# Kernel tuning notes

Hardware: AMD Instinct MI355X
Metric: run time of the kernel (lower is better)

The kernel has to match this reference:

```python
import jax, jax.numpy as jnp
import numpy as np

B, S, D, H = 2, 2048, 1024, 16
HD = D // H  # 64
SCALE = float(np.sqrt(HD))


def setup_inputs() -> dict:
    key = jax.random.key(0)
    ks = jax.random.split(key, 11)
    def lin(kw, kb, fan_in):
        bound = 1.0 / np.sqrt(fan_in)
        W = jax.random.uniform(kw, (D, D), jnp.float32, -bound, bound)
        b = jax.random.uniform(kb, (D,), jnp.float32, -bound, bound)
        return W, b
    Wq, bq = lin(ks[0], ks[1], D)
    Wk, bk = lin(ks[2], ks[3], D)
    Wv, bv = lin(ks[4], ks[5], D)
    Wo, bo = lin(ks[6], ks[7], D)
    q = jax.random.normal(ks[8], (B, S, D), jnp.float32)
    k = jax.random.normal(ks[9], (B, S, D), jnp.float32)
    v = jax.random.normal(ks[10], (B, S, D), jnp.float32)
    mask = jnp.ones((B, 1, S, S), jnp.int32)
    return {"q": q, "k": k, "v": v, "mask": mask,
            "Wq": Wq, "bq": bq, "Wk": Wk, "bk": bk,
            "Wv": Wv, "bv": bv, "Wo": Wo, "bo": bo}


def reference(q, k, v, mask, Wq, bq, Wk, bk, Wv, bv, Wo, bo):
    # torch Linear: x @ W.T + b
    def proj(x, W, b):
        y = x @ W.T + b                      # [B,S,D]
        return y.reshape(B, -1, H, HD).transpose(0, 2, 1, 3)  # [B,H,S,HD]
    Q = proj(q, Wq, bq)
    K = proj(k, Wk, bk)
    V = proj(v, Wv, bv)
    scores = jnp.einsum('bhqd,bhkd->bhqk', Q, K) / SCALE     # [B,H,S,S]
    scores = jnp.where(mask == 0, -1e9, scores)
    attn = jax.nn.softmax(scores, axis=-1)                   # dropout in eval mode = identity
    out = jnp.einsum('bhqk,bhkd->bhqd', attn, V)             # [B,H,S,HD]
    out = out.transpose(0, 2, 1, 3).reshape(B, -1, D)        # [B,S,D]
    return out @ Wo.T + bo
```

## Files before the change

### kernel.cpp

```cpp
#include <hip/hip_runtime.h>
#include <math.h>

#define BB 2
#define SS 2048
#define DD 1024
#define HH 16
#define HDIM 64
#define KK 1024
#define MM 4096

#define QFOLD 0.18033688011112042f

typedef _Float16 f16x2 __attribute__((ext_vector_type(2)));
typedef _Float16 f16x4 __attribute__((ext_vector_type(4)));
typedef _Float16 f16x8 __attribute__((ext_vector_type(8)));
typedef float    f32x4 __attribute__((ext_vector_type(4)));

#define GLL16(gp, lp) __builtin_amdgcn_global_load_lds(                        \
    (const __attribute__((address_space(1))) void*)(gp),                       \
    (__attribute__((address_space(3))) void*)(lp), 16, 0, 0)

static __device__ __forceinline__ float fast_exp2(float x) {
    float r;
    asm("v_exp_f32 %0, %1" : "=v"(r) : "v"(x));
    return r;
}
static __device__ __forceinline__ f16x2 cvt_pk(float a, float b) {
    f16x2 r;
    asm("v_cvt_pkrtz_f16_f32 %0, %1, %2" : "=v"(r) : "v"(a), "v"(b));
    return r;
}

__global__ __launch_bounds__(256) void prep(
    const float* __restrict__ q,  const float* __restrict__ k,
    const float* __restrict__ v,  const float* __restrict__ wq,
    const float* __restrict__ wk, const float* __restrict__ wv,
    const float* __restrict__ wo, const int* __restrict__ mask,
    _Float16* __restrict__ qh,  _Float16* __restrict__ kh,
    _Float16* __restrict__ vh,  _Float16* __restrict__ wqh,
    _Float16* __restrict__ wkh, _Float16* __restrict__ wvh,
    _Float16* __restrict__ woh, unsigned short* __restrict__ bm16)
{
    if (blockIdx.x < 16384u) {
        const unsigned u  = blockIdx.x * 256u + threadIdx.x;
        const unsigned U1 = 1u << 20;
        const unsigned U2 = 1u << 18;
        const float* src; _Float16* dst; unsigned off;
        float sc = 1.0f;
        if (u < 3u * U1) {
            const unsigned t = u >> 20; off = u & (U1 - 1u);
            src = (t == 0) ? q  : (t == 1) ? k  : v;
            dst = (t == 0) ? qh : (t == 1) ? kh : vh;
        } else {
            const unsigned r = u - 3u * U1;
            const unsigned t = r >> 18; off = r & (U2 - 1u);
            src = (t == 0) ? wq  : (t == 1) ? wk  : (t == 2) ? wv  : wo;
            dst = (t == 0) ? wqh : (t == 1) ? wkh : (t == 2) ? wvh : woh;
            if (t == 0) sc = QFOLD;
        }
        const float4 x = ((const float4*)src)[off];
        f16x4 y;
        y[0] = (_Float16)(x.x * sc); y[1] = (_Float16)(x.y * sc);
        y[2] = (_Float16)(x.z * sc); y[3] = (_Float16)(x.w * sc);
        ((f16x4*)dst)[off] = y;
    } else {
        const size_t t = (size_t)(blockIdx.x - 16384u) * 256 + threadIdx.x;
        const int4* p = (const int4*)(mask + t * 16);
        const int4 a = p[0], b = p[1], c = p[2], d = p[3];
        unsigned vv = 0;
        vv |= (a.x != 0) << 0;  vv |= (a.y != 0) << 1;
        vv |= (a.z != 0) << 2;  vv |= (a.w != 0) << 3;
        vv |= (b.x != 0) << 4;  vv |= (b.y != 0) << 5;
        vv |= (b.z != 0) << 6;  vv |= (b.w != 0) << 7;
        vv |= (c.x != 0) << 8;  vv |= (c.y != 0) << 9;
        vv |= (c.z != 0) << 10; vv |= (c.w != 0) << 11;
        vv |= (d.x != 0) << 12; vv |= (d.y != 0) << 13;
        vv |= (d.z != 0) << 14; vv |= (d.w != 0) << 15;
        bm16[t] = (unsigned short)vv;
    }
}

#define GEMM_BODY(X, W)                                                        \
    __shared__ _Float16 As[128 * 32];                                          \
    __shared__ _Float16 Bs[64 * 32];                                           \
    const int tid  = threadIdx.x;                                              \
    const int lane = tid & 63;                                                 \
    const int lr   = lane & 15;                                                \
    const int lg   = lane >> 4;                                                \
    const int wave = tid >> 6;                                                 \
    const int wr   = wave >> 1;                                                \
    const int wc   = wave & 1;                                                 \
    const int m0 = blockIdx.y << 7;                                            \
    const int n0 = blockIdx.x << 6;                                            \
    const char* Xb = (const char*)(X);                                         \
    const char* Wb = (const char*)(W);                                         \
    const int pa0 = tid * 16;                                                  \
    const int pa1 = pa0 + 4096;                                                \
    const int ra0 = pa0 >> 6, ca0 = pa0 & 63;                                  \
    const int ra1 = pa1 >> 6, ca1 = pa1 & 63;                                  \
    const int rb0 = pa0 >> 6, cb0 = pa0 & 63;                                  \
    f32x4 acc[4][2] = {};                                                      \
    for (int k0 = 0; k0 < KK; k0 += 32) {                                      \
        GLL16(Xb + ((size_t)(m0 + ra0) * KK + k0) * 2 + ca0, (char*)As + pa0); \
        GLL16(Xb + ((size_t)(m0 + ra1) * KK + k0) * 2 + ca1, (char*)As + pa1); \
        GLL16(Wb + ((size_t)(n0 + rb0) * KK + k0) * 2 + cb0, (char*)Bs + pa0); \
        __syncthreads();                                                       \
        f16x8 af[4], bf[2];                                                    \
        _Pragma("unroll")                                                      \
        for (int mi = 0; mi < 4; ++mi)                                         \
            af[mi] = *(const f16x8*)((const char*)As +                         \
                       ((wr * 64 + mi * 16 + lr) * 64 + lg * 16));             \
        _Pragma("unroll")                                                      \
        for (int ni = 0; ni < 2; ++ni)                                         \
            bf[ni] = *(const f16x8*)((const char*)Bs +                         \
                       ((wc * 32 + ni * 16 + lr) * 64 + lg * 16));             \
        _Pragma("unroll")                                                      \
        for (int mi = 0; mi < 4; ++mi)                                         \
            _Pragma("unroll")                                                  \
            for (int ni = 0; ni < 2; ++ni)                                     \
                acc[mi][ni] = __builtin_amdgcn_mfma_f32_16x16x32_f16(          \
                    af[mi], bf[ni], acc[mi][ni], 0, 0, 0);                     \
        __syncthreads();                                                       \
    }

__global__ __launch_bounds__(256) void gemm_qkv(
    const _Float16* __restrict__ qx, const _Float16* __restrict__ kx,
    const _Float16* __restrict__ vx,
    const _Float16* __restrict__ wqh, const _Float16* __restrict__ wkh,
    const _Float16* __restrict__ wvh,
    const float* __restrict__ bq, const float* __restrict__ bk,
    const float* __restrict__ bv,
    _Float16* __restrict__ Qh, _Float16* __restrict__ Kh,
    _Float16* __restrict__ Vt)
{
    const int z = blockIdx.z;
    const _Float16* X = (z == 0) ? qx : (z == 1) ? kx : vx;
    const _Float16* W = (z == 0) ? wqh : (z == 1) ? wkh : wvh;
    const float* bias = (z == 0) ? bq : (z == 1) ? bk : bv;
    const float bsc   = (z == 0) ? QFOLD : 1.0f;
    _Float16* Yh      = (z == 0) ? Qh : Kh;

    GEMM_BODY(X, W)

    #pragma unroll
    for (int ni = 0; ni < 2; ++ni) {
        const int n  = n0 + wc * 32 + ni * 16 + lr;
        const float bv_ = bias[n] * bsc;
        #pragma unroll
        for (int mi = 0; mi < 4; ++mi) {
            const int mbase = m0 + wr * 64 + mi * 16 + lg * 4;
            if (z < 2) {
                #pragma unroll
                for (int r = 0; r < 4; ++r) {
                    const int m = mbase + r;
                    const int b_ = m >> 11, s_ = m & (SS - 1);
                    const int h_ = n >> 6,  d_ = n & (HDIM - 1);
                    Yh[(((size_t)(b_ * HH + h_)) * SS + s_) * HDIM + d_] =
                        (_Float16)(acc[mi][ni][r] + bv_);
                }
            } else {
                const int b_ = mbase >> 11, s_ = mbase & (SS - 1);
                const int h_ = n >> 6,      d_ = n & (HDIM - 1);
                f16x4 tv;
                #pragma unroll
                for (int r = 0; r < 4; ++r) tv[r] = (_Float16)(acc[mi][ni][r] + bv_);
                *(f16x4*)(Vt + (((size_t)(b_ * HH + h_)) * HDIM + d_) * SS + s_) = tv;
            }
        }
    }
}

__global__ __launch_bounds__(256) void gemm_out(
    const _Float16* __restrict__ X, const _Float16* __restrict__ W,
    const float* __restrict__ bias, float* __restrict__ Y)
{
    GEMM_BODY(X, W)

    #pragma unroll
    for (int ni = 0; ni < 2; ++ni) {
        const int n  = n0 + wc * 32 + ni * 16 + lr;
        const float bv_ = bias[n];
        #pragma unroll
        for (int mi = 0; mi < 4; ++mi) {
            const int mbase = m0 + wr * 64 + mi * 16 + lg * 4;
            #pragma unroll
            for (int r = 0; r < 4; ++r)
                Y[(size_t)(mbase + r) * DD + n] = acc[mi][ni][r] + bv_;
        }
    }
}

__global__ __launch_bounds__(256) void attn_mfma4(
    const _Float16* __restrict__ Qh, const _Float16* __restrict__ Kh,
    const _Float16* __restrict__ Vt, const unsigned long long* __restrict__ bm,
    _Float16* __restrict__ AO)
{
    __shared__ _Float16 KbufS[2][4096];
    __shared__ _Float16 VbufS[2][4096];

    const int tid  = threadIdx.x;
    const int lane = tid & 63;
    const int wq   = tid >> 6;
    const int bh   = blockIdx.x;
    const int b_   = bh >> 4;
    const int h_   = bh & (HH - 1);
    const int q0   = blockIdx.y << 7;
    const int lr   = lane & 15;
    const int lg   = lane >> 4;

    const int qrowA = q0 + wq * 32 + lr;
    const int qrowB = qrowA + 16;
    const _Float16* qbA = Qh + ((size_t)bh * SS + qrowA) * HDIM;
    const _Float16* qbB = Qh + ((size_t)bh * SS + qrowB) * HDIM;
    const f16x8 qfA0 = *(const f16x8*)(qbA + lg * 8);
    const f16x8 qfA1 = *(const f16x8*)(qbA + 32 + lg * 8);
    const f16x8 qfB0 = *(const f16x8*)(qbB + lg * 8);
    const f16x8 qfB1 = *(const f16x8*)(qbB + 32 + lg * 8);

    const int c0 = tid, c1 = tid + 256;
    const int kr0 = c0 >> 3, krc0 = (c0 & 7) ^ (kr0 & 7);
    const int kr1 = c1 >> 3, krc1 = (c1 & 7) ^ (kr1 & 7);
    const _Float16* gK0 = Kh + ((size_t)bh * SS + kr0) * HDIM + krc0 * 8;
    const _Float16* gK1 = Kh + ((size_t)bh * SS + kr1) * HDIM + krc1 * 8;
    const _Float16* gV0 = Vt + ((size_t)bh * HDIM + kr0) * SS + krc0 * 8;
    const _Float16* gV1 = Vt + ((size_t)bh * HDIM + kr1) * SS + krc1 * 8;
    const int woff = (tid >> 6) << 10;

    float mA = -INFINITY, mB = -INFINITY;
    f32x4 oaccA[4], oaccB[4];
    #pragma unroll
    for (int dc = 0; dc < 4; ++dc) {
        oaccA[dc] = (f32x4){0.f, 0.f, 0.f, 0.f};
        oaccB[dc] = (f32x4){0.f, 0.f, 0.f, 0.f};
    }
    f32x4 laccA = (f32x4){0.f, 0.f, 0.f, 0.f};
    f32x4 laccB = (f32x4){0.f, 0.f, 0.f, 0.f};

    f16x8 ones;
    #pragma unroll
    for (int e = 0; e < 8; ++e) ones[e] = (_Float16)1.0f;

    const unsigned long long* bmrowA = bm + ((size_t)b_ * SS + qrowA) * (SS / 64);
    const unsigned long long* bmrowB = bm + ((size_t)b_ * SS + qrowB) * (SS / 64);

#define STAGE(KT, BSEL) do {                                                   \
    GLL16(gK0 + (size_t)(KT) * HDIM, (char*)KbufS[BSEL] + woff);               \
    GLL16(gK1 + (size_t)(KT) * HDIM, (char*)KbufS[BSEL] + 4096 + woff);        \
    GLL16(gV0 + (KT), (char*)VbufS[BSEL] + woff);                              \
    GLL16(gV1 + (KT), (char*)VbufS[BSEL] + 4096 + woff);                       \
  } while (0)

    STAGE(0, 0);
    __syncthreads();

    const int xk0 = ((lg       ^ (lr & 7)) << 4);
    const int xk1 = (((4 + lg) ^ (lr & 7)) << 4);
    const int xv  = ((lr & 7) << 4);

    unsigned long long bmA = bmrowA[0];
    unsigned long long bmB = bmrowB[0];

    for (int t = 0; t < SS / 64; ++t) {
        const int cur = t & 1;
        if (t < SS / 64 - 1) STAGE((t + 1) * 64, cur ^ 1);
        unsigned long long bmA_n = 0, bmB_n = 0;
        if (t < SS / 64 - 1) { bmA_n = bmrowA[t + 1]; bmB_n = bmrowB[t + 1]; }

        const char* kb = (const char*)KbufS[cur];
        const char* vb = (const char*)VbufS[cur];

        f32x4 sA[4], sB[4];
        __builtin_amdgcn_s_setprio(1);
        #pragma unroll
        for (int kg = 0; kg < 4; ++kg) {
            const char* rp = kb + (kg * 16 + lr) * 128;
            const f16x8 kf0 = *(const f16x8*)(rp + xk0);
            const f16x8 kf1 = *(const f16x8*)(rp + xk1);
            f32x4 a = (f32x4){0.f, 0.f, 0.f, 0.f};
            a = __builtin_amdgcn_mfma_f32_16x16x32_f16(kf0, qfA0, a, 0, 0, 0);
            a = __builtin_amdgcn_mfma_f32_16x16x32_f16(kf1, qfA1, a, 0, 0, 0);
            sA[kg] = a;
            f32x4 b2 = (f32x4){0.f, 0.f, 0.f, 0.f};
            b2 = __builtin_amdgcn_mfma_f32_16x16x32_f16(kf0, qfB0, b2, 0, 0, 0);
            b2 = __builtin_amdgcn_mfma_f32_16x16x32_f16(kf1, qfB1, b2, 0, 0, 0);
            sB[kg] = b2;
        }
        __builtin_amdgcn_s_setprio(0);

        float svA[16], svB[16];
        #pragma unroll
        for (int kg = 0; kg < 4; ++kg)
            #pragma unroll
            for (int r = 0; r < 4; ++r) {
                svA[kg * 4 + r] = sA[kg][r];
                svB[kg * 4 + r] = sB[kg][r];
            }

        if (~bmA) {
            #pragma unroll
            for (int kg = 0; kg < 4; ++kg)
                #pragma unroll
                for (int r = 0; r < 4; ++r)
                    if (!((bmA >> (kg * 16 + lg * 4 + r)) & 1ull))
                        svA[kg * 4 + r] = -1e9f;
        }
        if (~bmB) {
            #pragma unroll
            for (int kg = 0; kg < 4; ++kg)
                #pragma unroll
                for (int r = 0; r < 4; ++r)
                    if (!((bmB >> (kg * 16 + lg * 4 + r)) & 1ull))
                        svB[kg * 4 + r] = -1e9f;
        }
        bmA = bmA_n; bmB = bmB_n;

        float pmA = svA[0], pmB = svB[0];
        #pragma unroll
        for (int i = 1; i < 16; ++i) {
            pmA = fmaxf(pmA, svA[i]);
            pmB = fmaxf(pmB, svB[i]);
        }
        pmA = fmaxf(pmA, __shfl_xor(pmA, 16));
        pmA = fmaxf(pmA, __shfl_xor(pmA, 32));
        pmB = fmaxf(pmB, __shfl_xor(pmB, 16));
        pmB = fmaxf(pmB, __shfl_xor(pmB, 32));

        if (!__all(pmA <= mA + 8.0f)) {
            const float m_new = fmaxf(mA, pmA);
            const float corr  = fast_exp2(mA - m_new);
            #pragma unroll
            for (int dc = 0; dc < 4; ++dc) oaccA[dc] *= corr;
            laccA *= corr;
            mA = m_new;
        }
        if (!__all(pmB <= mB + 8.0f)) {
            const float m_new = fmaxf(mB, pmB);
            const float corr  = fast_exp2(mB - m_new);
            #pragma unroll
            for (int dc = 0; dc < 4; ++dc) oaccB[dc] *= corr;
            laccB *= corr;
            mB = m_new;
        }

        float pA[16], pB[16];
        #pragma unroll
        for (int i = 0; i < 16; ++i) {
            pA[i] = fast_exp2(svA[i] - mA);
            pB[i] = fast_exp2(svB[i] - mB);
        }

        union { f16x2 h2[4]; f16x8 v8; } uA0, uA1, uB0, uB1;
        #pragma unroll
        for (int e = 0; e < 4; ++e) {
            uA0.h2[e] = cvt_pk(pA[2 * e],     pA[2 * e + 1]);
            uA1.h2[e] = cvt_pk(pA[8 + 2 * e], pA[9 + 2 * e]);
            uB0.h2[e] = cvt_pk(pB[2 * e],     pB[2 * e + 1]);
            uB1.h2[e] = cvt_pk(pB[8 + 2 * e], pB[9 + 2 * e]);
        }
        const f16x8 pbA0 = uA0.v8, pbA1 = uA1.v8;
        const f16x8 pbB0 = uB0.v8, pbB1 = uB1.v8;

        __builtin_amdgcn_s_setprio(1);
        #pragma unroll
        for (int dc = 0; dc < 4; ++dc) {
            const char* rp = vb + (dc * 16 + lr) * 128;
            const f16x4 a0 = *(const f16x4*)(rp + ((0  + lg * 8) ^ xv));
            const f16x4 a1 = *(const f16x4*)(rp + ((32 + lg * 8) ^ xv));
            const f16x4 a2 = *(const f16x4*)(rp + ((64 + lg * 8) ^ xv));
            const f16x4 a3 = *(const f16x4*)(rp + ((96 + lg * 8) ^ xv));
            const f16x8 va0 = __builtin_shufflevector(a0, a1, 0, 1, 2, 3, 4, 5, 6, 7);
            const f16x8 va1 = __builtin_shufflevector(a2, a3, 0, 1, 2, 3, 4, 5, 6, 7);
            oaccA[dc] = __builtin_amdgcn_mfma_f32_16x16x32_f16(va0, pbA0, oaccA[dc], 0, 0, 0);
            oaccA[dc] = __builtin_amdgcn_mfma_f32_16x16x32_f16(va1, pbA1, oaccA[dc], 0, 0, 0);
            oaccB[dc] = __builtin_amdgcn_mfma_f32_16x16x32_f16(va0, pbB0, oaccB[dc], 0, 0, 0);
            oaccB[dc] = __builtin_amdgcn_mfma_f32_16x16x32_f16(va1, pbB1, oaccB[dc], 0, 0, 0);
        }
        laccA = __builtin_amdgcn_mfma_f32_16x16x32_f16(ones, pbA0, laccA, 0, 0, 0);
        laccA = __builtin_amdgcn_mfma_f32_16x16x32_f16(ones, pbA1, laccA, 0, 0, 0);
        laccB = __builtin_amdgcn_mfma_f32_16x16x32_f16(ones, pbB0, laccB, 0, 0, 0);
        laccB = __builtin_amdgcn_mfma_f32_16x16x32_f16(ones, pbB1, laccB, 0, 0, 0);
        __builtin_amdgcn_s_setprio(0);
        __syncthreads();
    }
#undef STAGE

    const float invlA = 1.0f / laccA[0];
    const float invlB = 1.0f / laccB[0];
    _Float16* obA = AO + ((size_t)b_ * SS + qrowA) * DD + h_ * HDIM;
    _Float16* obB = AO + ((size_t)b_ * SS + qrowB) * DD + h_ * HDIM;
    #pragma unroll
    for (int dc = 0; dc < 4; ++dc) {
        f16x4 rA, rB;
        #pragma unroll
        for (int r = 0; r < 4; ++r) {
            rA[r] = (_Float16)(oaccA[dc][r] * invlA);
            rB[r] = (_Float16)(oaccB[dc][r] * invlB);
        }
        *reinterpret_cast<f16x4*>(obA + dc * 16 + lg * 4) = rA;
        *reinterpret_cast<f16x4*>(obB + dc * 16 + lg * 4) = rB;
    }
}

extern "C" void kernel_launch(void* const* d_in, const int* in_sizes, int n_in,
                              void* d_out, int out_size, void* d_ws, size_t ws_size,
                              hipStream_t stream)
{
    const float* q    = (const float*)d_in[0];
    const float* k    = (const float*)d_in[1];
    const float* v    = (const float*)d_in[2];
    const int*   mask = (const int*)d_in[3];
    const float* Wq   = (const float*)d_in[4];
    const float* bq   = (const float*)d_in[5];
    const float* Wk   = (const float*)d_in[6];
    const float* bk   = (const float*)d_in[7];
    const float* Wv   = (const float*)d_in[8];
    const float* bv   = (const float*)d_in[9];
    const float* Wo   = (const float*)d_in[10];
    const float* bo   = (const float*)d_in[11];
    float* out = (float*)d_out;

    char* w = (char*)d_ws;
    _Float16* qx  = (_Float16*)(w);
    _Float16* kx  = (_Float16*)(w + 8  * 1048576);
    _Float16* vx  = (_Float16*)(w + 16 * 1048576);
    _Float16* wqh = (_Float16*)(w + 24 * 1048576);
    _Float16* wkh = (_Float16*)(w + 26 * 1048576);
    _Float16* wvh = (_Float16*)(w + 28 * 1048576);
    _Float16* woh = (_Float16*)(w + 30 * 1048576);
    _Float16* Qh  = (_Float16*)(w + 32 * 1048576);
    _Float16* Kh  = (_Float16*)(w + 40 * 1048576);
    _Float16* Vt  = (_Float16*)(w + 48 * 1048576);
    unsigned long long* bm = (unsigned long long*)(w + 56 * 1048576);
    _Float16* AO  = (_Float16*)(w);

    prep<<<18432, 256, 0, stream>>>(q, k, v, Wq, Wk, Wv, Wo, mask,
                                    qx, kx, vx, wqh, wkh, wvh, woh,
                                    (unsigned short*)bm);

    const dim3 gqkv(DD / 64, MM / 128, 3);
    gemm_qkv<<<gqkv, 256, 0, stream>>>(qx, kx, vx, wqh, wkh, wvh,
                                       bq, bk, bv, Qh, Kh, Vt);

    const dim3 gattn(BB * HH, SS / 128);
    attn_mfma4<<<gattn, 256, 0, stream>>>(Qh, Kh, Vt, bm, AO);

    const dim3 gout(DD / 64, MM / 128);
    gemm_out<<<gout, 256, 0, stream>>>(AO, woh, bo, out);
}
```

Before: 167.6 us.

## Split attention key range across two blocks and merge with log-sum-exp combine kernel

```diff
diff --git a/kernel.cpp b/kernel.cpp
--- a/kernel.cpp
+++ b/kernel.cpp
@@ -8,6 +8,7 @@
 #define HDIM 64
 #define KK 1024
 #define MM 4096
+#define KSPLIT 2
 
 #define QFOLD 0.18033688011112042f
 
@@ -23,6 +24,11 @@
 static __device__ __forceinline__ float fast_exp2(float x) {
     float r;
     asm("v_exp_f32 %0, %1" : "=v"(r) : "v"(x));
+    return r;
+}
+static __device__ __forceinline__ float fast_log2(float x) {
+    float r;
+    asm("v_log_f32 %0, %1" : "=v"(r) : "v"(x));
     return r;
 }
 static __device__ __forceinline__ f16x2 cvt_pk(float a, float b) {
@@ -190,10 +196,10 @@
     }
 }
 
-__global__ __launch_bounds__(256) void attn_mfma4(
+__global__ __launch_bounds__(256) void attn_mfma5(
     const _Float16* __restrict__ Qh, const _Float16* __restrict__ Kh,
     const _Float16* __restrict__ Vt, const unsigned long long* __restrict__ bm,
-    _Float16* __restrict__ AO)
+    _Float16* __restrict__ Opart, float* __restrict__ Lpart)
 {
     __shared__ _Float16 KbufS[2][4096];
     __shared__ _Float16 VbufS[2][4096];
@@ -203,10 +209,13 @@
     const int wq   = tid >> 6;
     const int bh   = blockIdx.x;
     const int b_   = bh >> 4;
-    const int h_   = bh & (HH - 1);
     const int q0   = blockIdx.y << 7;
+    const int ks   = blockIdx.z;
     const int lr   = lane & 15;
     const int lg   = lane >> 4;
+
+    const int NT = SS / 64 / KSPLIT;
+    const int t0 = ks * NT;
 
     const int qrowA = q0 + wq * 32 + lr;
     const int qrowB = qrowA + 16;
@@ -250,21 +259,22 @@
     GLL16(gV1 + (KT), (char*)VbufS[BSEL] + 4096 + woff);                       \
   } while (0)
 
-    STAGE(0, 0);
+    STAGE(t0 * 64, 0);
     __syncthreads();
 
     const int xk0 = ((lg       ^ (lr & 7)) << 4);
     const int xk1 = (((4 + lg) ^ (lr & 7)) << 4);
     const int xv  = ((lr & 7) << 4);
 
-    unsigned long long bmA = bmrowA[0];
-    unsigned long long bmB = bmrowB[0];
-
-    for (int t = 0; t < SS / 64; ++t) {
-        const int cur = t & 1;
-        if (t < SS / 64 - 1) STAGE((t + 1) * 64, cur ^ 1);
+    unsigned long long bmA = bmrowA[t0];
+    unsigned long long bmB = bmrowB[t0];
+
+    for (int ti = 0; ti < NT; ++ti) {
+        const int t = t0 + ti;
+        const int cur = ti & 1;
+        if (ti < NT - 1) STAGE((t + 1) * 64, cur ^ 1);
         unsigned long long bmA_n = 0, bmB_n = 0;
-        if (t < SS / 64 - 1) { bmA_n = bmrowA[t + 1]; bmB_n = bmrowB[t + 1]; }
+        if (ti < NT - 1) { bmA_n = bmrowA[t + 1]; bmB_n = bmrowB[t + 1]; }
 
         const char* kb = (const char*)KbufS[cur];
         const char* vb = (const char*)VbufS[cur];
@@ -384,10 +394,16 @@
     }
 #undef STAGE
 
+    _Float16* Op = Opart + (size_t)ks * (BB * HH) * SS * HDIM;
+    float*    Lp = Lpart + (size_t)ks * (BB * HH) * SS;
+
     const float invlA = 1.0f / laccA[0];
     const float invlB = 1.0f / laccB[0];
-    _Float16* obA = AO + ((size_t)b_ * SS + qrowA) * DD + h_ * HDIM;
-    _Float16* obB = AO + ((size_t)b_ * SS + qrowB) * DD + h_ * HDIM;
+    const float LA_ = mA + fast_log2(laccA[0]);
+    const float LB_ = mB + fast_log2(laccB[0]);
+
+    _Float16* opA = Op + ((size_t)bh * SS + qrowA) * HDIM;
+    _Float16* opB = Op + ((size_t)bh * SS + qrowB) * HDIM;
     #pragma unroll
     for (int dc = 0; dc < 4; ++dc) {
         f16x4 rA, rB;
@@ -396,9 +412,39 @@
             rA[r] = (_Float16)(oaccA[dc][r] * invlA);
             rB[r] = (_Float16)(oaccB[dc][r] * invlB);
         }
-        *reinterpret_cast<f16x4*>(obA + dc * 16 + lg * 4) = rA;
-        *reinterpret_cast<f16x4*>(obB + dc * 16 + lg * 4) = rB;
-    }
+        *reinterpret_cast<f16x4*>(opA + dc * 16 + lg * 4) = rA;
+        *reinterpret_cast<f16x4*>(opB + dc * 16 + lg * 4) = rB;
+    }
+    if (lg == 0) {
+        Lp[(size_t)bh * SS + qrowA] = LA_;
+        Lp[(size_t)bh * SS + qrowB] = LB_;
+    }
+}
+
+__global__ __launch_bounds__(256) void combine(
+    const _Float16* __restrict__ Opart, const float* __restrict__ Lpart,
+    _Float16* __restrict__ AO)
+{
+    const int tid = threadIdx.x;
+    const int row = blockIdx.x * 32 + (tid >> 3);
+    const int dc  = (tid & 7) * 8;
+    const int bh = row >> 11, s = row & (SS - 1);
+    const int b_ = bh >> 4,   h_ = bh & (HH - 1);
+    const size_t PER = (size_t)(BB * HH) * SS;
+
+    const float L0 = Lpart[row], L1 = Lpart[PER + row];
+    const float Ls = fmaxf(L0, L1);
+    const float w0 = fast_exp2(L0 - Ls);
+    const float w1 = fast_exp2(L1 - Ls);
+    const float inv = 1.0f / (w0 + w1);
+
+    const f16x8 a = *(const f16x8*)(Opart + (size_t)row * HDIM + dc);
+    const f16x8 b = *(const f16x8*)(Opart + PER * HDIM + (size_t)row * HDIM + dc);
+    f16x8 r;
+    #pragma unroll
+    for (int i = 0; i < 8; ++i)
+        r[i] = (_Float16)(((float)a[i] * w0 + (float)b[i] * w1) * inv);
+    *(f16x8*)(AO + ((size_t)b_ * SS + s) * DD + h_ * HDIM + dc) = r;
 }
 
 extern "C" void kernel_launch(void* const* d_in, const int* in_sizes, int n_in,
@@ -431,7 +477,9 @@
     _Float16* Kh  = (_Float16*)(w + 40 * 1048576);
     _Float16* Vt  = (_Float16*)(w + 48 * 1048576);
     unsigned long long* bm = (unsigned long long*)(w + 56 * 1048576);
-    _Float16* AO  = (_Float16*)(w);
+    _Float16* Opart = (_Float16*)(w + 8 * 1048576);
+    float*    Lpart = (float*)(w + 24 * 1048576);
+    _Float16* AO    = (_Float16*)(w);
 
     prep<<<18432, 256, 0, stream>>>(q, k, v, Wq, Wk, Wv, Wo, mask,
                                     qx, kx, vx, wqh, wkh, wvh, woh,
@@ -441,8 +489,10 @@
     gemm_qkv<<<gqkv, 256, 0, stream>>>(qx, kx, vx, wqh, wkh, wvh,
                                        bq, bk, bv, Qh, Kh, Vt);
 
-    const dim3 gattn(BB * HH, SS / 128);
-    attn_mfma4<<<gattn, 256, 0, stream>>>(Qh, Kh, Vt, bm, AO);
+    const dim3 gattn(BB * HH, SS / 128, KSPLIT);
+    attn_mfma5<<<gattn, 256, 0, stream>>>(Qh, Kh, Vt, bm, Opart, Lpart);
+
+    combine<<<2048, 256, 0, stream>>>(Opart, Lpart, AO);
 
     const dim3 gout(DD / 64, MM / 128);
     gemm_out<<<gout, 256, 0, stream>>>(AO, woh, bo, out);
```

Result: slower. 175.5 us (+4.7%).

## Switch attention kernel to 32x32x16 MFMA tiles with permlane32 P-fragment reshuffle

Applied to the files above, without the earlier changes.

```diff
diff --git a/kernel.cpp b/kernel.cpp
--- a/kernel.cpp
+++ b/kernel.cpp
@@ -15,6 +15,8 @@
 typedef _Float16 f16x4 __attribute__((ext_vector_type(4)));
 typedef _Float16 f16x8 __attribute__((ext_vector_type(8)));
 typedef float    f32x4 __attribute__((ext_vector_type(4)));
+typedef float    f32x16 __attribute__((ext_vector_type(16)));
+typedef unsigned uint2v __attribute__((ext_vector_type(2)));
 
 #define GLL16(gp, lp) __builtin_amdgcn_global_load_lds(                        \
     (const __attribute__((address_space(1))) void*)(gp),                       \
@@ -25,10 +27,10 @@
     asm("v_exp_f32 %0, %1" : "=v"(r) : "v"(x));
     return r;
 }
-static __device__ __forceinline__ f16x2 cvt_pk(float a, float b) {
-    f16x2 r;
-    asm("v_cvt_pkrtz_f16_f32 %0, %1, %2" : "=v"(r) : "v"(a), "v"(b));
-    return r;
+static __device__ __forceinline__ unsigned cvt_pk_u(float a, float b) {
+    union { f16x2 h; unsigned u; } r;
+    asm("v_cvt_pkrtz_f16_f32 %0, %1, %2" : "=v"(r.h) : "v"(a), "v"(b));
+    return r.u;
 }
 
 __global__ __launch_bounds__(256) void prep(
@@ -190,7 +192,7 @@
     }
 }
 
-__global__ __launch_bounds__(256) void attn_mfma4(
+__global__ __launch_bounds__(256) void attn_mfma7(
     const _Float16* __restrict__ Qh, const _Float16* __restrict__ Kh,
     const _Float16* __restrict__ Vt, const unsigned long long* __restrict__ bm,
     _Float16* __restrict__ AO)
@@ -205,17 +207,15 @@
     const int b_   = bh >> 4;
     const int h_   = bh & (HH - 1);
     const int q0   = blockIdx.y << 7;
-    const int lr   = lane & 15;
-    const int lg   = lane >> 4;
-
-    const int qrowA = q0 + wq * 32 + lr;
-    const int qrowB = qrowA + 16;
-    const _Float16* qbA = Qh + ((size_t)bh * SS + qrowA) * HDIM;
-    const _Float16* qbB = Qh + ((size_t)bh * SS + qrowB) * HDIM;
-    const f16x8 qfA0 = *(const f16x8*)(qbA + lg * 8);
-    const f16x8 qfA1 = *(const f16x8*)(qbA + 32 + lg * 8);
-    const f16x8 qfB0 = *(const f16x8*)(qbB + lg * 8);
-    const f16x8 qfB1 = *(const f16x8*)(qbB + 32 + lg * 8);
+    const int lq   = lane & 31;
+    const int hi   = lane >> 5;
+
+    const int qrow = q0 + wq * 32 + lq;
+    const _Float16* qbase = Qh + ((size_t)bh * SS + qrow) * HDIM;
+    f16x8 qf[4];
+    #pragma unroll
+    for (int j = 0; j < 4; ++j)
+        qf[j] = *(const f16x8*)(qbase + j * 16 + hi * 8);
 
     const int c0 = tid, c1 = tid + 256;
     const int kr0 = c0 >> 3, krc0 = (c0 & 7) ^ (kr0 & 7);
@@ -226,22 +226,12 @@
     const _Float16* gV1 = Vt + ((size_t)bh * HDIM + kr1) * SS + krc1 * 8;
     const int woff = (tid >> 6) << 10;
 
-    float mA = -INFINITY, mB = -INFINITY;
-    f32x4 oaccA[4], oaccB[4];
+    float m_run = -INFINITY, l_run = 0.f;
+    f32x16 oacc0, oacc1;
     #pragma unroll
-    for (int dc = 0; dc < 4; ++dc) {
-        oaccA[dc] = (f32x4){0.f, 0.f, 0.f, 0.f};
-        oaccB[dc] = (f32x4){0.f, 0.f, 0.f, 0.f};
-    }
-    f32x4 laccA = (f32x4){0.f, 0.f, 0.f, 0.f};
-    f32x4 laccB = (f32x4){0.f, 0.f, 0.f, 0.f};
-
-    f16x8 ones;
-    #pragma unroll
-    for (int e = 0; e < 8; ++e) ones[e] = (_Float16)1.0f;
-
-    const unsigned long long* bmrowA = bm + ((size_t)b_ * SS + qrowA) * (SS / 64);
-    const unsigned long long* bmrowB = bm + ((size_t)b_ * SS + qrowB) * (SS / 64);
+    for (int i = 0; i < 16; ++i) { oacc0[i] = 0.f; oacc1[i] = 0.f; }
+
+    const unsigned long long* bmrow = bm + ((size_t)b_ * SS + qrow) * (SS / 64);
 
 #define STAGE(KT, BSEL) do {                                                   \
     GLL16(gK0 + (size_t)(KT) * HDIM, (char*)KbufS[BSEL] + woff);               \
@@ -253,151 +243,115 @@
     STAGE(0, 0);
     __syncthreads();
 
-    const int xk0 = ((lg       ^ (lr & 7)) << 4);
-    const int xk1 = (((4 + lg) ^ (lr & 7)) << 4);
-    const int xv  = ((lr & 7) << 4);
-
-    unsigned long long bmA = bmrowA[0];
-    unsigned long long bmB = bmrowB[0];
+    const int kxor = lq & 7;
+    unsigned long long bmv = bmrow[0];
 
     for (int t = 0; t < SS / 64; ++t) {
         const int cur = t & 1;
         if (t < SS / 64 - 1) STAGE((t + 1) * 64, cur ^ 1);
-        unsigned long long bmA_n = 0, bmB_n = 0;
-        if (t < SS / 64 - 1) { bmA_n = bmrowA[t + 1]; bmB_n = bmrowB[t + 1]; }
+        unsigned long long bmv_n = 0;
+        if (t < SS / 64 - 1) bmv_n = bmrow[t + 1];
 
         const char* kb = (const char*)KbufS[cur];
         const char* vb = (const char*)VbufS[cur];
 
-        f32x4 sA[4], sB[4];
+        f32x16 s0, s1;
+        #pragma unroll
+        for (int i = 0; i < 16; ++i) { s0[i] = 0.f; s1[i] = 0.f; }
         __builtin_amdgcn_s_setprio(1);
         #pragma unroll
-        for (int kg = 0; kg < 4; ++kg) {
-            const char* rp = kb + (kg * 16 + lr) * 128;
-            const f16x8 kf0 = *(const f16x8*)(rp + xk0);
-            const f16x8 kf1 = *(const f16x8*)(rp + xk1);
-            f32x4 a = (f32x4){0.f, 0.f, 0.f, 0.f};
-            a = __builtin_amdgcn_mfma_f32_16x16x32_f16(kf0, qfA0, a, 0, 0, 0);
-            a = __builtin_amdgcn_mfma_f32_16x16x32_f16(kf1, qfA1, a, 0, 0, 0);
-            sA[kg] = a;
-            f32x4 b2 = (f32x4){0.f, 0.f, 0.f, 0.f};
-            b2 = __builtin_amdgcn_mfma_f32_16x16x32_f16(kf0, qfB0, b2, 0, 0, 0);
-            b2 = __builtin_amdgcn_mfma_f32_16x16x32_f16(kf1, qfB1, b2, 0, 0, 0);
-            sB[kg] = b2;
+        for (int j = 0; j < 4; ++j) {
+            const char* kp = kb + lq * 128 + (((2 * j + hi) ^ kxor) << 4);
+            const f16x8 k0 = *(const f16x8*)(kp);
+            const f16x8 k1 = *(const f16x8*)(kp + 4096);
+            s0 = __builtin_amdgcn_mfma_f32_32x32x16_f16(k0, qf[j], s0, 0, 0, 0);
+            s1 = __builtin_amdgcn_mfma_f32_32x32x16_f16(k1, qf[j], s1, 0, 0, 0);
         }
         __builtin_amdgcn_s_setprio(0);
 
-        float svA[16], svB[16];
-        #pragma unroll
-        for (int kg = 0; kg < 4; ++kg)
+        float sv[32];
+        #pragma unroll
+        for (int r = 0; r < 16; ++r) { sv[r] = s0[r]; sv[16 + r] = s1[r]; }
+
+        if (~bmv) {
+            const unsigned long long bsh = bmv >> (hi * 4);
             #pragma unroll
-            for (int r = 0; r < 4; ++r) {
-                svA[kg * 4 + r] = sA[kg][r];
-                svB[kg * 4 + r] = sB[kg][r];
+            for (int r = 0; r < 16; ++r) {
+                const int crow = (r & 3) + 8 * (r >> 2);
+                if (!((bsh >> crow) & 1ull))        sv[r]      = -1e9f;
+                if (!((bsh >> (32 + crow)) & 1ull)) sv[16 + r] = -1e9f;
             }
-
-        if (~bmA) {
+        }
+        bmv = bmv_n;
+
+        float pmax = sv[0];
+        #pragma unroll
+        for (int i = 1; i < 32; ++i) pmax = fmaxf(pmax, sv[i]);
+        pmax = fmaxf(pmax, __shfl_xor(pmax, 32));
+
+        if (!__all(pmax <= m_run + 8.0f)) {
+            const float m_new = fmaxf(m_run, pmax);
+            const float corr  = fast_exp2(m_run - m_new);
+            oacc0 *= corr; oacc1 *= corr;
+            l_run *= corr;
+            m_run = m_new;
+        }
+
+        float psum = 0.f;
+        #pragma unroll
+        for (int i = 0; i < 32; ++i) { sv[i] = fast_exp2(sv[i] - m_run); psum += sv[i]; }
+        psum += __shfl_xor(psum, 32);
+        l_run += psum;
+
+        f16x8 Bf[2][2];
+        #pragma unroll
+        for (int kt2 = 0; kt2 < 2; ++kt2) {
             #pragma unroll
-            for (int kg = 0; kg < 4; ++kg)
-                #pragma unroll
-                for (int r = 0; r < 4; ++r)
-                    if (!((bmA >> (kg * 16 + lg * 4 + r)) & 1ull))
-                        svA[kg * 4 + r] = -1e9f;
-        }
-        if (~bmB) {
+            for (int kh = 0; kh < 2; ++kh) {
+                const int bse = 16 * kt2 + 8 * kh;
+                unsigned u0 = cvt_pk_u(sv[bse + 0], sv[bse + 1]);
+                unsigned u1 = cvt_pk_u(sv[bse + 2], sv[bse + 3]);
+                unsigned u2 = cvt_pk_u(sv[bse + 4], sv[bse + 5]);
+                unsigned u3 = cvt_pk_u(sv[bse + 6], sv[bse + 7]);
+                const uint2v r02 = __builtin_amdgcn_permlane32_swap(u0, u2, false, false);
+                const uint2v r13 = __builtin_amdgcn_permlane32_swap(u1, u3, false, false);
+                union { unsigned w[4]; f16x8 v; } bu;
+                bu.w[0] = r02[0]; bu.w[1] = r13[0];
+                bu.w[2] = r02[1]; bu.w[3] = r13[1];
+                Bf[kt2][kh] = bu.v;
+            }
+        }
+
+        __builtin_amdgcn_s_setprio(1);
+        #pragma unroll
+        for (int kt2 = 0; kt2 < 2; ++kt2) {
             #pragma unroll
-            for (int kg = 0; kg < 4; ++kg)
-                #pragma unroll
-                for (int r = 0; r < 4; ++r)
-                    if (!((bmB >> (kg * 16 + lg * 4 + r)) & 1ull))
-                        svB[kg * 4 + r] = -1e9f;
-        }
-        bmA = bmA_n; bmB = bmB_n;
-
-        float pmA = svA[0], pmB = svB[0];
-        #pragma unroll
-        for (int i = 1; i < 16; ++i) {
-            pmA = fmaxf(pmA, svA[i]);
-            pmB = fmaxf(pmB, svB[i]);
-        }
-        pmA = fmaxf(pmA, __shfl_xor(pmA, 16));
-        pmA = fmaxf(pmA, __shfl_xor(pmA, 32));
-        pmB = fmaxf(pmB, __shfl_xor(pmB, 16));
-        pmB = fmaxf(pmB, __shfl_xor(pmB, 32));
-
-        if (!__all(pmA <= mA + 8.0f)) {
-            const float m_new = fmaxf(mA, pmA);
-            const float corr  = fast_exp2(mA - m_new);
-            #pragma unroll
-            for (int dc = 0; dc < 4; ++dc) oaccA[dc] *= corr;
-            laccA *= corr;
-            mA = m_new;
-        }
-        if (!__all(pmB <= mB + 8.0f)) {
-            const float m_new = fmaxf(mB, pmB);
-            const float corr  = fast_exp2(mB - m_new);
-            #pragma unroll
-            for (int dc = 0; dc < 4; ++dc) oaccB[dc] *= corr;
-            laccB *= corr;
-            mB = m_new;
-        }
-
-        float pA[16], pB[16];
-        #pragma unroll
-        for (int i = 0; i < 16; ++i) {
-            pA[i] = fast_exp2(svA[i] - mA);
-            pB[i] = fast_exp2(svB[i] - mB);
-        }
-
-        union { f16x2 h2[4]; f16x8 v8; } uA0, uA1, uB0, uB1;
-        #pragma unroll
-        for (int e = 0; e < 4; ++e) {
-            uA0.h2[e] = cvt_pk(pA[2 * e],     pA[2 * e + 1]);
-            uA1.h2[e] = cvt_pk(pA[8 + 2 * e], pA[9 + 2 * e]);
-            uB0.h2[e] = cvt_pk(pB[2 * e],     pB[2 * e + 1]);
-            uB1.h2[e] = cvt_pk(pB[8 + 2 * e], pB[9 + 2 * e]);
-        }
-        const f16x8 pbA0 = uA0.v8, pbA1 = uA1.v8;
-        const f16x8 pbB0 = uB0.v8, pbB1 = uB1.v8;
-
-        __builtin_amdgcn_s_setprio(1);
-        #pragma unroll
-        for (int dc = 0; dc < 4; ++dc) {
-            const char* rp = vb + (dc * 16 + lr) * 128;
-            const f16x4 a0 = *(const f16x4*)(rp + ((0  + lg * 8) ^ xv));
-            const f16x4 a1 = *(const f16x4*)(rp + ((32 + lg * 8) ^ xv));
-            const f16x4 a2 = *(const f16x4*)(rp + ((64 + lg * 8) ^ xv));
-            const f16x4 a3 = *(const f16x4*)(rp + ((96 + lg * 8) ^ xv));
-            const f16x8 va0 = __builtin_shufflevector(a0, a1, 0, 1, 2, 3, 4, 5, 6, 7);
-            const f16x8 va1 = __builtin_shufflevector(a2, a3, 0, 1, 2, 3, 4, 5, 6, 7);
-            oaccA[dc] = __builtin_amdgcn_mfma_f32_16x16x32_f16(va0, pbA0, oaccA[dc], 0, 0, 0);
-            oaccA[dc] = __builtin_amdgcn_mfma_f32_16x16x32_f16(va1, pbA1, oaccA[dc], 0, 0, 0);
-            oaccB[dc] = __builtin_amdgcn_mfma_f32_16x16x32_f16(va0, pbB0, oaccB[dc], 0, 0, 0);
-            oaccB[dc] = __builtin_amdgcn_mfma_f32_16x16x32_f16(va1, pbB1, oaccB[dc], 0, 0, 0);
-        }
-        laccA = __builtin_amdgcn_mfma_f32_16x16x32_f16(ones, pbA0, laccA, 0, 0, 0);
-        laccA = __builtin_amdgcn_mfma_f32_16x16x32_f16(ones, pbA1, laccA, 0, 0, 0);
-        laccB = __builtin_amdgcn_mfma_f32_16x16x32_f16(ones, pbB0, laccB, 0, 0, 0);
-        laccB = __builtin_amdgcn_mfma_f32_16x16x32_f16(ones, pbB1, laccB, 0, 0, 0);
+            for (int kh = 0; kh < 2; ++kh) {
+                const int chunk = kt2 * 4 + kh * 2 + hi;
+                const int coff  = ((chunk ^ kxor) << 4);
+                const f16x8 v0 = *(const f16x8*)(vb + lq * 128 + coff);
+                const f16x8 v1 = *(const f16x8*)(vb + (32 + lq) * 128 + coff);
+                oacc0 = __builtin_amdgcn_mfma_f32_32x32x16_f16(v0, Bf[kt2][kh], oacc0, 0, 0, 0);
+                oacc1 = __builtin_amdgcn_mfma_f32_32x32x16_f16(v1, Bf[kt2][kh], oacc1, 0, 0, 0);
+            }
+        }
         __builtin_amdgcn_s_setprio(0);
         __syncthreads();
     }
 #undef STAGE
 
-    const float invlA = 1.0f / laccA[0];
-    const float invlB = 1.0f / laccB[0];
-    _Float16* obA = AO + ((size_t)b_ * SS + qrowA) * DD + h_ * HDIM;
-    _Float16* obB = AO + ((size_t)b_ * SS + qrowB) * DD + h_ * HDIM;
+    const float invl = 1.0f / l_run;
+    _Float16* ob = AO + ((size_t)b_ * SS + qrow) * DD + h_ * HDIM + 4 * hi;
     #pragma unroll
-    for (int dc = 0; dc < 4; ++dc) {
-        f16x4 rA, rB;
-        #pragma unroll
-        for (int r = 0; r < 4; ++r) {
-            rA[r] = (_Float16)(oaccA[dc][r] * invlA);
-            rB[r] = (_Float16)(oaccB[dc][r] * invlB);
-        }
-        *reinterpret_cast<f16x4*>(obA + dc * 16 + lg * 4) = rA;
-        *reinterpret_cast<f16x4*>(obB + dc * 16 + lg * 4) = rB;
+    for (int g = 0; g < 4; ++g) {
+        f16x4 r0, r1;
+        #pragma unroll
+        for (int tt = 0; tt < 4; ++tt) {
+            r0[tt] = (_Float16)(oacc0[4 * g + tt] * invl);
+            r1[tt] = (_Float16)(oacc1[4 * g + tt] * invl);
+        }
+        *(f16x4*)(ob + 8 * g)      = r0;
+        *(f16x4*)(ob + 32 + 8 * g) = r1;
     }
 }
 
@@ -442,7 +396,7 @@
                                        bq, bk, bv, Qh, Kh, Vt);
 
     const dim3 gattn(BB * HH, SS / 128);
-    attn_mfma4<<<gattn, 256, 0, stream>>>(Qh, Kh, Vt, bm, AO);
+    attn_mfma7<<<gattn, 256, 0, stream>>>(Qh, Kh, Vt, bm, AO);
 
     const dim3 gout(DD / 64, MM / 128);
     gemm_out<<<gout, 256, 0, stream>>>(AO, woh, bo, out);
```

Measured after the change: 159.5 us. 4.9% less time.
